# Kernel tuning notes

Measured on AMD Instinct MI355X. Metric: run time of the kernel, lower is better.

## Reference

```python
import jax, jax.numpy as jnp
import numpy as np

N, T, C = 100000, 12, 32  # nodes, periods, hidden (A3TGCN out_channels hardcoded 32)
E = 3_200_000


def setup_inputs() -> dict:
    key = jax.random.key(0)
    ks = jax.random.split(key, 20)
    s_g = 1.0 / np.sqrt(1.0)        # GCNConv glorot-ish for in=1
    s_l = 1.0 / np.sqrt(2.0 * C)    # torch Linear default for in=2C
    s_h = 1.0 / np.sqrt(C)
    u = lambda k, shape, s: jax.random.uniform(k, shape, jnp.float32, -s, s)
    return {
        "x": jax.random.normal(ks[0], (N, T), jnp.float32),
        "edge_index": jax.random.randint(ks[1], (2, E), 0, N, jnp.int32),
        "edge_weight": jax.random.uniform(ks[2], (E,), jnp.float32),
        # TGCN gate GCNConv params (in_channels=1, out=C)
        "w_z": u(ks[3], (1, C), s_g), "b_z": jnp.zeros((C,), jnp.float32),
        "w_r": u(ks[4], (1, C), s_g), "b_r": jnp.zeros((C,), jnp.float32),
        "w_h": u(ks[5], (1, C), s_g), "b_h": jnp.zeros((C,), jnp.float32),
        # TGCN gate Linear params (torch layout [out=C, in=2C])
        "lw_z": u(ks[6], (C, 2 * C), s_l), "lb_z": u(ks[7], (C,), s_l),
        "lw_r": u(ks[8], (C, 2 * C), s_l), "lb_r": u(ks[9], (C,), s_l),
        "lw_h": u(ks[10], (C, 2 * C), s_l), "lb_h": u(ks[11], (C,), s_l),
        # A3TGCN temporal attention
        "att": jax.random.uniform(ks[12], (T,), jnp.float32),
        # head Linear(32, 1)
        "head_w": u(ks[13], (1, C), s_h), "head_b": u(ks[14], (1,), s_h),
    }


def reference(x, edge_index, edge_weight, w_z, b_z, w_r, b_r, w_h, b_h,
              lw_z, lb_z, lw_r, lb_r, lw_h, lb_h, att, head_w, head_b):
    n = x.shape[0]
    # --- GCN normalization with self-loops (fill value 1) ---
    loop = jnp.arange(n)
    s = jnp.concatenate([edge_index[0], loop])
    d = jnp.concatenate([edge_index[1], loop])
    w = jnp.concatenate([edge_weight, jnp.ones((n,), edge_weight.dtype)])
    deg = jax.ops.segment_sum(w, d, num_segments=n)
    dinv = jnp.where(deg > 0, jax.lax.rsqrt(deg), 0.0)
    norm = dinv[s] * w * dinv[d]
    # --- shared sparse aggregation: A_hat @ X for all periods at once ---
    # in_channels = 1, so GCNConv(X_t) = (A_hat x_t) * W + b; aggregate scalars [N,T]
    agg = jax.ops.segment_sum(norm[:, None] * x[s], d, num_segments=n)  # [N, T]
    # gate convolutions, [N, T, C]
    cz = agg[:, :, None] * w_z[0] + b_z
    ch = agg[:, :, None] * w_h[0] + b_h
    # A3TGCN passes H=None every period -> hidden starts at 0 each step, so
    # linear([conv, H]) reduces to conv @ W[:, :C].T + b, and the reset gate R
    # multiplies H=0 (no effect on output).
    Z = jax.nn.sigmoid(jnp.einsum('ntc,oc->nto', cz, lw_z[:, :C]) + lb_z)
    Ht = jnp.tanh(jnp.einsum('ntc,oc->nto', ch, lw_h[:, :C]) + lb_h)
    Hp = (1.0 - Z) * Ht  # per-period hidden state, [N, T, C]
    probs = jax.nn.softmax(att)
    h = jnp.einsum('t,ntc->nc', probs, Hp)  # attention-weighted temporal sum
    h = jax.nn.relu(h)
    return h @ head_w.T + head_b  # [N, 1]
```

## Files before the change

### kernel.cpp

```cpp
#include <hip/hip_runtime.h>
#include <hip/hip_fp16.h>

#define N_NODES 100000
#define T_P 12
#define C_H 32
#define E_EDGES 3200000

#define NODES_PER_B 256
#define NB 391
#define CAPA 8704

#define VEC_E (E_EDGES / 4)
#define P1_THREADS 512
#define P1_VECS 2048
#define NBLK1 ((VEC_E + P1_VECS - 1) / P1_VECS)


__global__ void params_kernel(const float* __restrict__ wz, const float* __restrict__ bz,
                              const float* __restrict__ wh, const float* __restrict__ bh,
                              const float* __restrict__ lwz, const float* __restrict__ lbz,
                              const float* __restrict__ lwh, const float* __restrict__ lbh,
                              const float* __restrict__ att, float* __restrict__ P,
                              int* __restrict__ cursor) {
    int o = threadIdx.x;
    if (o < NB) cursor[o] = 0;
    if (o < C_H) {
        float az = 0.f, bzv = 0.f, ah = 0.f, bhv = 0.f;
        for (int c = 0; c < C_H; ++c) {
            float lz = lwz[o * 2 * C_H + c];
            float lh = lwh[o * 2 * C_H + c];
            az += wz[c] * lz;  bzv += bz[c] * lz;
            ah += wh[c] * lh;  bhv += bh[c] * lh;
        }
        P[16 + o]  = az;  P[48 + o]  = bzv + lbz[o];
        P[80 + o]  = ah;  P[112 + o] = bhv + lbh[o];
    }
    if (o == 0) {
        float m = -1e30f;
        for (int t = 0; t < T_P; ++t) m = fmaxf(m, att[t]);
        float e[T_P], s = 0.f;
        for (int t = 0; t < T_P; ++t) { e[t] = __expf(att[t] - m); s += e[t]; }
        float inv = 1.0f / s;
        for (int t = 0; t < T_P; ++t) P[t] = e[t] * inv;
    }
}

__global__ void __launch_bounds__(512)
bucket_scatter_kernel(const int* __restrict__ src, const int* __restrict__ dst,
                      const float* __restrict__ w, int* __restrict__ cursor,
                      float2* __restrict__ entries) {
    __shared__ int h[NB];
    __shared__ int claim[NB];
    int tid = threadIdx.x;
    int vbase = blockIdx.x * P1_VECS;
    for (int i = tid; i < NB; i += 512) h[i] = 0;
    __syncthreads();
    const int4* d4 = (const int4*)dst;
    int rra[16];
#pragma unroll
    for (int q = 0; q < 4; ++q) {
        int v = vbase + q * 512 + tid;
        if (v < VEC_E) {
            int4 d = d4[v];
            rra[q * 4 + 0] = atomicAdd(&h[d.x >> 8], 1);
            rra[q * 4 + 1] = atomicAdd(&h[d.y >> 8], 1);
            rra[q * 4 + 2] = atomicAdd(&h[d.z >> 8], 1);
            rra[q * 4 + 3] = atomicAdd(&h[d.w >> 8], 1);
        }
    }
    __syncthreads();
    for (int i = tid; i < NB; i += 512) {
        int c = h[i];
        claim[i] = c ? atomicAdd(&cursor[i], c) : 0;
    }
    __syncthreads();
    const int4* s4 = (const int4*)src;
    const float4* w4 = (const float4*)w;
#pragma unroll
    for (int q = 0; q < 4; ++q) {
        int v = vbase + q * 512 + tid;
        if (v < VEC_E) {
            int4 d = d4[v];
            int4 s = s4[v];
            float4 ww = w4[v];
            int bin, dl, pos;
            bin = d.x >> 8; dl = d.x & 255; pos = claim[bin] + rra[q * 4 + 0];
            if (pos < CAPA) entries[(size_t)bin * CAPA + pos] = make_float2(__int_as_float(s.x | (dl << 17)), ww.x);
            bin = d.y >> 8; dl = d.y & 255; pos = claim[bin] + rra[q * 4 + 1];
            if (pos < CAPA) entries[(size_t)bin * CAPA + pos] = make_float2(__int_as_float(s.y | (dl << 17)), ww.y);
            bin = d.z >> 8; dl = d.z & 255; pos = claim[bin] + rra[q * 4 + 2];
            if (pos < CAPA) entries[(size_t)bin * CAPA + pos] = make_float2(__int_as_float(s.z | (dl << 17)), ww.z);
            bin = d.w >> 8; dl = d.w & 255; pos = claim[bin] + rra[q * 4 + 3];
            if (pos < CAPA) entries[(size_t)bin * CAPA + pos] = make_float2(__int_as_float(s.w | (dl << 17)), ww.w);
        }
    }
}

__global__ void __launch_bounds__(1024)
prep_kernel(const float2* __restrict__ entries, const int* __restrict__ cursor,
            const float* __restrict__ x, float* __restrict__ dinv, __half* __restrict__ y) {
    __shared__ float wsum[NODES_PER_B];
    __shared__ float dloc[NODES_PER_B];
    int tid = threadIdx.x;
    int b = blockIdx.x;
    int nbase = b << 8;
    size_t lo = (size_t)b * CAPA;
    int ne = cursor[b]; if (ne > CAPA) ne = CAPA;
    if (tid < NODES_PER_B) wsum[tid] = 0.f;
    __syncthreads();
    for (int k = tid; k < ne; k += 1024) {
        float2 e = entries[lo + k];
        atomicAdd(&wsum[(__float_as_int(e.x) >> 17) & 255], e.y);
    }
    __syncthreads();
    if (tid < NODES_PER_B) {
        int n = nbase + tid;
        float di = (n < N_NODES) ? rsqrtf(1.0f + wsum[tid]) : 0.f;
        dloc[tid] = di;
        if (n < N_NODES) dinv[n] = di;
    }
    __syncthreads();
    if (tid < 512) {
        int nl = tid >> 1, q = tid & 1;
        int n = nbase + nl;
        if (n < N_NODES) {
            float di = dloc[nl];
            union { __half h[8]; float4 f4; } u;
            if (q == 0) {
                float4 a = ((const float4*)x)[(size_t)n * 3 + 0];
                float4 c = ((const float4*)x)[(size_t)n * 3 + 1];
                u.h[0] = __float2half_rn(a.x * di); u.h[1] = __float2half_rn(a.y * di);
                u.h[2] = __float2half_rn(a.z * di); u.h[3] = __float2half_rn(a.w * di);
                u.h[4] = __float2half_rn(c.x * di); u.h[5] = __float2half_rn(c.y * di);
                u.h[6] = __float2half_rn(c.z * di); u.h[7] = __float2half_rn(c.w * di);
            } else {
                float4 c = ((const float4*)x)[(size_t)n * 3 + 2];
                u.h[0] = __float2half_rn(c.x * di); u.h[1] = __float2half_rn(c.y * di);
                u.h[2] = __float2half_rn(c.z * di); u.h[3] = __float2half_rn(c.w * di);
                u.h[4] = __ushort_as_half((unsigned short)0);
                u.h[5] = __ushort_as_half((unsigned short)0);
                u.h[6] = __ushort_as_half((unsigned short)0);
                u.h[7] = __ushort_as_half((unsigned short)0);
            }
            ((float4*)y)[((size_t)n << 1) + q] = u.f4;
        }
    }
}

__global__ void __launch_bounds__(1024, 8)
sort_gather_kernel(const float2* __restrict__ entries, const int* __restrict__ cursor,
                   const float* __restrict__ dinv, const __half* __restrict__ y,
                   const float* __restrict__ P, const float* __restrict__ head_w,
                   const float* __restrict__ head_b, float* __restrict__ out) {
    __shared__ float2 stage[CAPA];
    __shared__ int   cnt[NODES_PER_B];
    __shared__ int   inc[NODES_PER_B];
    __shared__ float Ps[160];
    __shared__ float hws[C_H];
    int tid = threadIdx.x;
    int b = blockIdx.x;
    size_t lo = (size_t)b * CAPA;
    int ne = cursor[b]; if (ne > CAPA) ne = CAPA;
    if (tid < 160) Ps[tid] = P[tid];
    if (tid < C_H) hws[tid] = head_w[tid];
    if (tid < NODES_PER_B) cnt[tid] = 0;
    __syncthreads();
    float2 ent[9];
    int    rr[9];
#pragma unroll
    for (int i = 0; i < 9; ++i) {
        int k = tid + i * 1024;
        if (k < ne) {
            float2 e = entries[lo + k];
            ent[i] = e;
            rr[i] = atomicAdd(&cnt[(__float_as_int(e.x) >> 17) & 255], 1);
        }
    }
    __syncthreads();
    if (tid < NODES_PER_B) inc[tid] = cnt[tid];
    __syncthreads();
    for (int d = 1; d < NODES_PER_B; d <<= 1) {
        int t = (tid >= d && tid < NODES_PER_B) ? inc[tid - d] : 0;
        __syncthreads();
        if (tid < NODES_PER_B) inc[tid] += t;
        __syncthreads();
    }
#pragma unroll
    for (int i = 0; i < 9; ++i) {
        int k = tid + i * 1024;
        if (k < ne) {
            int dl = (__float_as_int(ent[i].x) >> 17) & 255;
            stage[inc[dl] - cnt[dl] + rr[i]] = ent[i];
        }
    }
    __syncthreads();
    int nl = tid >> 2, lane = tid & 3;
    int n = (b << 8) + nl;
    if (n >= N_NODES) return;
    int end = inc[nl];
    int start = end - cnt[nl];
    float4 a0 = make_float4(0.f, 0.f, 0.f, 0.f);
    float4 a1 = a0, a2 = a0;
    if (lane == 0) {
        const float4* yn = (const float4*)(y + ((size_t)n << 4));
        float4 r0 = yn[0], r1 = yn[1];
        const __half2* hp = (const __half2*)&r0;
        const __half2* hq = (const __half2*)&r1;
        float2 p0 = __half22float2(hp[0]), p1 = __half22float2(hp[1]);
        float2 p2 = __half22float2(hp[2]), p3 = __half22float2(hp[3]);
        float2 p4 = __half22float2(hq[0]), p5 = __half22float2(hq[1]);
        a0 = make_float4(p0.x, p0.y, p1.x, p1.y);
        a1 = make_float4(p2.x, p2.y, p3.x, p3.y);
        a2 = make_float4(p4.x, p4.y, p5.x, p5.y);
    }
    for (int j = start + lane; j < end; j += 4) {
        float2 e = stage[j];
        int s = __float_as_int(e.x) & 0x1FFFF;
        float c = e.y;
        const float4* ys = (const float4*)(y + ((size_t)s << 4));
        float4 r0 = ys[0], r1 = ys[1];
        const __half2* hp = (const __half2*)&r0;
        const __half2* hq = (const __half2*)&r1;
        float2 p0 = __half22float2(hp[0]), p1 = __half22float2(hp[1]);
        float2 p2 = __half22float2(hp[2]), p3 = __half22float2(hp[3]);
        float2 p4 = __half22float2(hq[0]), p5 = __half22float2(hq[1]);
        a0.x += c * p0.x; a0.y += c * p0.y; a0.z += c * p1.x; a0.w += c * p1.y;
        a1.x += c * p2.x; a1.y += c * p2.y; a1.z += c * p3.x; a1.w += c * p3.y;
        a2.x += c * p4.x; a2.y += c * p4.y; a2.z += c * p5.x; a2.w += c * p5.y;
    }
#define RED4(v) v += __shfl_xor(v, 1); v += __shfl_xor(v, 2)
    RED4(a0.x); RED4(a0.y); RED4(a0.z); RED4(a0.w);
    RED4(a1.x); RED4(a1.y); RED4(a1.z); RED4(a1.w);
    RED4(a2.x); RED4(a2.y); RED4(a2.z); RED4(a2.w);
#undef RED4
    float din = dinv[n];
    float av[T_P];
    av[0] = a0.x * din; av[1] = a0.y * din; av[2]  = a0.z * din; av[3]  = a0.w * din;
    av[4] = a1.x * din; av[5] = a1.y * din; av[6]  = a1.z * din; av[7]  = a1.w * din;
    av[8] = a2.x * din; av[9] = a2.y * din; av[10] = a2.z * din; av[11] = a2.w * din;
    float acc = 0.f;
#pragma unroll
    for (int k = 0; k < 8; ++k) {
        int c = (lane << 3) + k;
        float Az = Ps[16 + c], Bz = Ps[48 + c], Ah = Ps[80 + c], Bh = Ps[112 + c];
        float hc = 0.f;
#pragma unroll
        for (int t = 0; t < T_P; ++t) {
            float a = av[t];
            float oz = 1.f / (1.f + __expf(a * Az + Bz));
            float vv = a * Ah + Bh;
            float th = 1.f - 2.f / (1.f + __expf(2.f * vv));
            hc += Ps[t] * oz * th;
        }
        acc += fmaxf(hc, 0.f) * hws[c];
    }
    acc += __shfl_xor(acc, 1);
    acc += __shfl_xor(acc, 2);
    if (lane == 0) out[n] = acc + head_b[0];
}

extern "C" void kernel_launch(void* const* d_in, const int* in_sizes, int n_in,
                              void* d_out, int out_size, void* d_ws, size_t ws_size,
                              hipStream_t stream) {
    const float* x    = (const float*)d_in[0];
    const int*   ei   = (const int*)d_in[1];
    const float* ew   = (const float*)d_in[2];
    const float* w_z  = (const float*)d_in[3];
    const float* b_z  = (const float*)d_in[4];
    const float* w_h  = (const float*)d_in[7];
    const float* b_h  = (const float*)d_in[8];
    const float* lw_z = (const float*)d_in[9];
    const float* lb_z = (const float*)d_in[10];
    const float* lw_h = (const float*)d_in[13];
    const float* lb_h = (const float*)d_in[14];
    const float* att  = (const float*)d_in[15];
    const float* hw   = (const float*)d_in[16];
    const float* hb   = (const float*)d_in[17];
    float* out = (float*)d_out;

    float* wsf      = (float*)d_ws;
    float* P        = wsf;
    float* dinv     = P + 256;
    int*   cursor   = (int*)(dinv + N_NODES);
    __half* y       = (__half*)(wsf + 100656);
    float2* entries = (float2*)(wsf + 100656 + (size_t)N_NODES * 8);

    const int* srcp = ei;
    const int* dstp = ei + E_EDGES;

    params_kernel<<<1, 1024, 0, stream>>>(w_z, b_z, w_h, b_h, lw_z, lb_z, lw_h, lb_h,
                                          att, P, cursor);
    bucket_scatter_kernel<<<NBLK1, P1_THREADS, 0, stream>>>(srcp, dstp, ew, cursor, entries);
    prep_kernel<<<NB, 1024, 0, stream>>>(entries, cursor, x, dinv, y);
    sort_gather_kernel<<<NB, 1024, 0, stream>>>(entries, cursor, dinv, y, P, hw, hb, out);
}
```

Before: 238.5 us.

## Halve bucket size, fp16-pack staged edges, recompute dinv in gather, fold params

Buckets now cover 128 nodes instead of 256, giving twice as many smaller blocks with 512 threads each. The sort stage packs each edge into a 32-bit record (17-bit source plus fp16 weight), which halves the shared staging buffer. It also recomputes the degree normalisation locally instead of reading a global dinv array. The separate params kernel becomes a memset plus work done in block 0 of prep, and the scatter reuses cached dst values instead of reloading them. Risks: fp16 edge weights lose precision, and the degree sum is now computed twice.

New measurement: 264.7 us. 1.11x slower.

```diff
diff --git a/kernel.cpp b/kernel.cpp
--- a/kernel.cpp
+++ b/kernel.cpp
@@ -6,44 +6,15 @@
 #define C_H 32
 #define E_EDGES 3200000
 
-#define NODES_PER_B 256
-#define NB 391
-#define CAPA 8704
+#define NODES_PER_B 128
+#define NB 782
+#define CAPA 4608
 
 #define VEC_E (E_EDGES / 4)
 #define P1_THREADS 512
 #define P1_VECS 2048
 #define NBLK1 ((VEC_E + P1_VECS - 1) / P1_VECS)
 
-
-__global__ void params_kernel(const float* __restrict__ wz, const float* __restrict__ bz,
-                              const float* __restrict__ wh, const float* __restrict__ bh,
-                              const float* __restrict__ lwz, const float* __restrict__ lbz,
-                              const float* __restrict__ lwh, const float* __restrict__ lbh,
-                              const float* __restrict__ att, float* __restrict__ P,
-                              int* __restrict__ cursor) {
-    int o = threadIdx.x;
-    if (o < NB) cursor[o] = 0;
-    if (o < C_H) {
-        float az = 0.f, bzv = 0.f, ah = 0.f, bhv = 0.f;
-        for (int c = 0; c < C_H; ++c) {
-            float lz = lwz[o * 2 * C_H + c];
-            float lh = lwh[o * 2 * C_H + c];
-            az += wz[c] * lz;  bzv += bz[c] * lz;
-            ah += wh[c] * lh;  bhv += bh[c] * lh;
-        }
-        P[16 + o]  = az;  P[48 + o]  = bzv + lbz[o];
-        P[80 + o]  = ah;  P[112 + o] = bhv + lbh[o];
-    }
-    if (o == 0) {
-        float m = -1e30f;
-        for (int t = 0; t < T_P; ++t) m = fmaxf(m, att[t]);
-        float e[T_P], s = 0.f;
-        for (int t = 0; t < T_P; ++t) { e[t] = __expf(att[t] - m); s += e[t]; }
-        float inv = 1.0f / s;
-        for (int t = 0; t < T_P; ++t) P[t] = e[t] * inv;
-    }
-}
 
 __global__ void __launch_bounds__(512)
 bucket_scatter_kernel(const int* __restrict__ src, const int* __restrict__ dst,
@@ -56,16 +27,18 @@
     for (int i = tid; i < NB; i += 512) h[i] = 0;
     __syncthreads();
     const int4* d4 = (const int4*)dst;
+    int4 dc[4];
     int rra[16];
 #pragma unroll
     for (int q = 0; q < 4; ++q) {
         int v = vbase + q * 512 + tid;
         if (v < VEC_E) {
             int4 d = d4[v];
-            rra[q * 4 + 0] = atomicAdd(&h[d.x >> 8], 1);
-            rra[q * 4 + 1] = atomicAdd(&h[d.y >> 8], 1);
-            rra[q * 4 + 2] = atomicAdd(&h[d.z >> 8], 1);
-            rra[q * 4 + 3] = atomicAdd(&h[d.w >> 8], 1);
+            dc[q] = d;
+            rra[q * 4 + 0] = atomicAdd(&h[d.x >> 7], 1);
+            rra[q * 4 + 1] = atomicAdd(&h[d.y >> 7], 1);
+            rra[q * 4 + 2] = atomicAdd(&h[d.z >> 7], 1);
+            rra[q * 4 + 3] = atomicAdd(&h[d.w >> 7], 1);
         }
     }
     __syncthreads();
@@ -80,47 +53,50 @@
     for (int q = 0; q < 4; ++q) {
         int v = vbase + q * 512 + tid;
         if (v < VEC_E) {
-            int4 d = d4[v];
+            int4 d = dc[q];
             int4 s = s4[v];
             float4 ww = w4[v];
             int bin, dl, pos;
-            bin = d.x >> 8; dl = d.x & 255; pos = claim[bin] + rra[q * 4 + 0];
+            bin = d.x >> 7; dl = d.x & 127; pos = claim[bin] + rra[q * 4 + 0];
             if (pos < CAPA) entries[(size_t)bin * CAPA + pos] = make_float2(__int_as_float(s.x | (dl << 17)), ww.x);
-            bin = d.y >> 8; dl = d.y & 255; pos = claim[bin] + rra[q * 4 + 1];
+            bin = d.y >> 7; dl = d.y & 127; pos = claim[bin] + rra[q * 4 + 1];
             if (pos < CAPA) entries[(size_t)bin * CAPA + pos] = make_float2(__int_as_float(s.y | (dl << 17)), ww.y);
-            bin = d.z >> 8; dl = d.z & 255; pos = claim[bin] + rra[q * 4 + 2];
+            bin = d.z >> 7; dl = d.z & 127; pos = claim[bin] + rra[q * 4 + 2];
             if (pos < CAPA) entries[(size_t)bin * CAPA + pos] = make_float2(__int_as_float(s.z | (dl << 17)), ww.z);
-            bin = d.w >> 8; dl = d.w & 255; pos = claim[bin] + rra[q * 4 + 3];
+            bin = d.w >> 7; dl = d.w & 127; pos = claim[bin] + rra[q * 4 + 3];
             if (pos < CAPA) entries[(size_t)bin * CAPA + pos] = make_float2(__int_as_float(s.w | (dl << 17)), ww.w);
         }
     }
 }
 
-__global__ void __launch_bounds__(1024)
+__global__ void __launch_bounds__(512)
 prep_kernel(const float2* __restrict__ entries, const int* __restrict__ cursor,
-            const float* __restrict__ x, float* __restrict__ dinv, __half* __restrict__ y) {
+            const float* __restrict__ x, __half* __restrict__ y,
+            const float* __restrict__ wz, const float* __restrict__ bz,
+            const float* __restrict__ wh, const float* __restrict__ bh,
+            const float* __restrict__ lwz, const float* __restrict__ lbz,
+            const float* __restrict__ lwh, const float* __restrict__ lbh,
+            const float* __restrict__ att, float* __restrict__ P) {
     __shared__ float wsum[NODES_PER_B];
     __shared__ float dloc[NODES_PER_B];
     int tid = threadIdx.x;
     int b = blockIdx.x;
-    int nbase = b << 8;
+    int nbase = b << 7;
     size_t lo = (size_t)b * CAPA;
     int ne = cursor[b]; if (ne > CAPA) ne = CAPA;
     if (tid < NODES_PER_B) wsum[tid] = 0.f;
     __syncthreads();
-    for (int k = tid; k < ne; k += 1024) {
+    for (int k = tid; k < ne; k += 512) {
         float2 e = entries[lo + k];
-        atomicAdd(&wsum[(__float_as_int(e.x) >> 17) & 255], e.y);
+        atomicAdd(&wsum[(__float_as_int(e.x) >> 17) & 127], e.y);
     }
     __syncthreads();
     if (tid < NODES_PER_B) {
         int n = nbase + tid;
-        float di = (n < N_NODES) ? rsqrtf(1.0f + wsum[tid]) : 0.f;
-        dloc[tid] = di;
-        if (n < N_NODES) dinv[n] = di;
-    }
-    __syncthreads();
-    if (tid < 512) {
+        dloc[tid] = (n < N_NODES) ? rsqrtf(1.0f + wsum[tid]) : 0.f;
+    }
+    __syncthreads();
+    if (tid < 256) {
         int nl = tid >> 1, q = tid & 1;
         int n = nbase + nl;
         if (n < N_NODES) {
@@ -145,16 +121,40 @@
             ((float4*)y)[((size_t)n << 1) + q] = u.f4;
         }
     }
+    if (b == 0) {
+        int o = tid;
+        if (o < C_H) {
+            float az = 0.f, bzv = 0.f, ah = 0.f, bhv = 0.f;
+            for (int c = 0; c < C_H; ++c) {
+                float lz = lwz[o * 2 * C_H + c];
+                float lh = lwh[o * 2 * C_H + c];
+                az += wz[c] * lz;  bzv += bz[c] * lz;
+                ah += wh[c] * lh;  bhv += bh[c] * lh;
+            }
+            P[16 + o]  = az;  P[48 + o]  = bzv + lbz[o];
+            P[80 + o]  = ah;  P[112 + o] = bhv + lbh[o];
+        }
+        if (o == 0) {
+            float m = -1e30f;
+            for (int t = 0; t < T_P; ++t) m = fmaxf(m, att[t]);
+            float e[T_P], s = 0.f;
+            for (int t = 0; t < T_P; ++t) { e[t] = __expf(att[t] - m); s += e[t]; }
+            float inv = 1.0f / s;
+            for (int t = 0; t < T_P; ++t) P[t] = e[t] * inv;
+        }
+    }
 }
 
-__global__ void __launch_bounds__(1024, 8)
+__global__ void __launch_bounds__(512, 8)
 sort_gather_kernel(const float2* __restrict__ entries, const int* __restrict__ cursor,
-                   const float* __restrict__ dinv, const __half* __restrict__ y,
-                   const float* __restrict__ P, const float* __restrict__ head_w,
-                   const float* __restrict__ head_b, float* __restrict__ out) {
-    __shared__ float2 stage[CAPA];
+                   const __half* __restrict__ y, const float* __restrict__ P,
+                   const float* __restrict__ head_w, const float* __restrict__ head_b,
+                   float* __restrict__ out) {
+    __shared__ unsigned int stage[CAPA];
     __shared__ int   cnt[NODES_PER_B];
     __shared__ int   inc[NODES_PER_B];
+    __shared__ float wsum[NODES_PER_B];
+    __shared__ float dloc[NODES_PER_B];
     __shared__ float Ps[160];
     __shared__ float hws[C_H];
     int tid = threadIdx.x;
@@ -163,17 +163,19 @@
     int ne = cursor[b]; if (ne > CAPA) ne = CAPA;
     if (tid < 160) Ps[tid] = P[tid];
     if (tid < C_H) hws[tid] = head_w[tid];
-    if (tid < NODES_PER_B) cnt[tid] = 0;
+    if (tid < NODES_PER_B) { cnt[tid] = 0; wsum[tid] = 0.f; }
     __syncthreads();
     float2 ent[9];
     int    rr[9];
 #pragma unroll
     for (int i = 0; i < 9; ++i) {
-        int k = tid + i * 1024;
+        int k = tid + i * 512;
         if (k < ne) {
             float2 e = entries[lo + k];
             ent[i] = e;
-            rr[i] = atomicAdd(&cnt[(__float_as_int(e.x) >> 17) & 255], 1);
+            int dl = (__float_as_int(e.x) >> 17) & 127;
+            rr[i] = atomicAdd(&cnt[dl], 1);
+            atomicAdd(&wsum[dl], e.y);
         }
     }
     __syncthreads();
@@ -185,17 +187,20 @@
         if (tid < NODES_PER_B) inc[tid] += t;
         __syncthreads();
     }
+    if (tid < NODES_PER_B) dloc[tid] = rsqrtf(1.0f + wsum[tid]);
 #pragma unroll
     for (int i = 0; i < 9; ++i) {
-        int k = tid + i * 1024;
+        int k = tid + i * 512;
         if (k < ne) {
-            int dl = (__float_as_int(ent[i].x) >> 17) & 255;
-            stage[inc[dl] - cnt[dl] + rr[i]] = ent[i];
+            int u = __float_as_int(ent[i].x);
+            int dl = (u >> 17) & 127;
+            unsigned int hb = (unsigned int)__half_as_ushort(__float2half_rn(ent[i].y));
+            stage[inc[dl] - cnt[dl] + rr[i]] = (unsigned int)(u & 0x1FFFF) | (hb << 17);
         }
     }
     __syncthreads();
     int nl = tid >> 2, lane = tid & 3;
-    int n = (b << 8) + nl;
+    int n = (b << 7) + nl;
     if (n >= N_NODES) return;
     int end = inc[nl];
     int start = end - cnt[nl];
@@ -214,9 +219,9 @@
         a2 = make_float4(p4.x, p4.y, p5.x, p5.y);
     }
     for (int j = start + lane; j < end; j += 4) {
-        float2 e = stage[j];
-        int s = __float_as_int(e.x) & 0x1FFFF;
-        float c = e.y;
+        unsigned int rec = stage[j];
+        int s = rec & 0x1FFFF;
+        float c = __half2float(__ushort_as_half((unsigned short)(rec >> 17)));
         const float4* ys = (const float4*)(y + ((size_t)s << 4));
         float4 r0 = ys[0], r1 = ys[1];
         const __half2* hp = (const __half2*)&r0;
@@ -233,7 +238,7 @@
     RED4(a1.x); RED4(a1.y); RED4(a1.z); RED4(a1.w);
     RED4(a2.x); RED4(a2.y); RED4(a2.z); RED4(a2.w);
 #undef RED4
-    float din = dinv[n];
+    float din = dloc[nl];
     float av[T_P];
     av[0] = a0.x * din; av[1] = a0.y * din; av[2]  = a0.z * din; av[3]  = a0.w * din;
     av[4] = a1.x * din; av[5] = a1.y * din; av[6]  = a1.z * din; av[7]  = a1.w * din;
@@ -280,17 +285,16 @@
 
     float* wsf      = (float*)d_ws;
     float* P        = wsf;
-    float* dinv     = P + 256;
-    int*   cursor   = (int*)(dinv + N_NODES);
-    __half* y       = (__half*)(wsf + 100656);
-    float2* entries = (float2*)(wsf + 100656 + (size_t)N_NODES * 8);
+    int*   cursor   = (int*)(wsf + 256);
+    __half* y       = (__half*)(wsf + 1040);
+    float2* entries = (float2*)(wsf + 1040 + (size_t)N_NODES * 8);
 
     const int* srcp = ei;
     const int* dstp = ei + E_EDGES;
 
-    params_kernel<<<1, 1024, 0, stream>>>(w_z, b_z, w_h, b_h, lw_z, lb_z, lw_h, lb_h,
-                                          att, P, cursor);
+    hipMemsetAsync(cursor, 0, NB * sizeof(int), stream);
     bucket_scatter_kernel<<<NBLK1, P1_THREADS, 0, stream>>>(srcp, dstp, ew, cursor, entries);
-    prep_kernel<<<NB, 1024, 0, stream>>>(entries, cursor, x, dinv, y);
-    sort_gather_kernel<<<NB, 1024, 0, stream>>>(entries, cursor, dinv, y, P, hw, hb, out);
+    prep_kernel<<<NB, 512, 0, stream>>>(entries, cursor, x, y,
+                                        w_z, b_z, w_h, b_h, lw_z, lb_z, lw_h, lb_h, att, P);
+    sort_gather_kernel<<<NB, 512, 0, stream>>>(entries, cursor, y, P, hw, hb, out);
 }
```
